# Kernel tuning notes

Measured on AMD Instinct MI355X. Metric: run time of the kernel, lower is better.

## Reference

```python
import jax, jax.numpy as jnp
import numpy as np

LAYER_SIZES = [1024, 1024, 1024, 1024, 1024, 1024, 512]
MAX_PATHS = 128
BATCH = 128
N_LAYERS = len(LAYER_SIZES) - 1


def setup_inputs() -> dict:
    key = jax.random.key(0)
    keys = jax.random.split(key, 1 + 2 * N_LAYERS)
    inp = {"x": jax.random.normal(keys[0], (BATCH, LAYER_SIZES[0]), dtype=jnp.float32)}
    for i in range(N_LAYERS):
        inp[f"W{i}"] = jax.random.normal(keys[1 + 2 * i], (LAYER_SIZES[i], LAYER_SIZES[i + 1]), dtype=jnp.float32) * 0.01
        inp[f"b{i}"] = jax.random.normal(keys[2 + 2 * i], (LAYER_SIZES[i + 1],), dtype=jnp.float32) * 0.01
    return inp


def _layer(data, W, b):
    # data: [B, in_feat, P] -> [B, out_feat, 3P]
    B, _, P = data.shape
    O = W.shape[1]
    pos = jnp.einsum('bfp,fo->bpo', data, W) + b          # [B, P, O]; neg branch is exactly -pos
    branches = jnp.stack([-pos, jnp.zeros_like(pos), pos], axis=-1)  # [B, P, O, 3]
    # transpose(1,2) then reshape: interleave branches per source path, matching torch
    return branches.transpose(0, 2, 1, 3).reshape(B, O, P * 3)


def _prune(data, keep):
    # keep top-`keep` paths by L2 norm over the feature dim
    norms = jnp.linalg.norm(data, axis=1)                 # [B, P]
    _, idx = jax.lax.top_k(norms, keep)                   # [B, keep]
    return jnp.take_along_axis(data, idx[:, None, :], axis=-1)


def _forward(x, Ws, bs):
    data = x[:, :, None]                                   # [B, F, 1]
    for i in range(N_LAYERS):
        data = _layer(data, Ws[i], bs[i])
        if i < N_LAYERS - 1:
            data = jnp.tanh(data)
        if data.shape[-1] > MAX_PATHS:
            data = _prune(data, MAX_PATHS)
    # collapse with 'max_abs': per (batch, feature) pick path with largest |value|
    idx = jnp.argmax(jnp.abs(data), axis=-1, keepdims=True)
    output = jnp.take_along_axis(data, idx, axis=-1).squeeze(-1)
    return output, data


def reference(x, W0, b0, W1, b1, W2, b2, W3, b3, W4, b4, W5, b5):
    Ws = [W0, W1, W2, W3, W4, W5]
    bs = [b0, b1, b2, b3, b4, b5]
    return _forward(x, Ws, bs)
```

## Files before the change

kernel.cpp:

```cpp
#include <hip/hip_runtime.h>
#include <math.h>


using s8v = __attribute__((ext_vector_type(8))) short;
using f4v = __attribute__((ext_vector_type(4))) float;

__device__ __forceinline__ float bf2f(short b) {
  unsigned u = ((unsigned)(unsigned short)b) << 16;
  return __builtin_bit_cast(float, u);
}
__device__ __forceinline__ short f2bf(float f) {
  unsigned u = __builtin_bit_cast(unsigned, f);
  u = (u + 0x7FFFu + ((u >> 16) & 1u)) >> 16;
  return (short)u;
}
__device__ __forceinline__ void split_store(float f, short* hi, short* lo) {
  short h = f2bf(f);
  *hi = h;
  *lo = f2bf(f - bf2f(h));
}

struct TWArgs {
  const float* W[6];
  short* Th[6];
  short* Tl[6];
};
__global__ void __launch_bounds__(256)
transW_all(TWArgs a, const float* __restrict__ x, short* __restrict__ A0h,
           short* __restrict__ A0l, float4* __restrict__ zreg) {
  __shared__ float tile[64][65];
  const int t = threadIdx.x;
  if (blockIdx.z == 6) {
    const int bf = blockIdx.y * 16 + blockIdx.x;
    if (bf < 128) {
      int i = (bf * 256 + t) * 4;
      float4 v = *(const float4*)&x[i];
      short4 h, l;
      h.x = f2bf(v.x); l.x = f2bf(v.x - bf2f(h.x));
      h.y = f2bf(v.y); l.y = f2bf(v.y - bf2f(h.y));
      h.z = f2bf(v.z); l.z = f2bf(v.z - bf2f(h.z));
      h.w = f2bf(v.w); l.w = f2bf(v.w - bf2f(h.w));
      *(short4*)&A0h[i] = h;
      *(short4*)&A0l[i] = l;
    } else {
      int flat = (bf - 128) * 256 + t;
      if (flat < 2976) {
        float4 zz = {0.f, 0.f, 0.f, 0.f};
        zreg[flat] = zz;
      }
    }
    return;
  }
  const int z = blockIdx.z;
  const int N = (z == 5) ? 512 : 1024;
  const int n0 = blockIdx.x * 64, k0 = blockIdx.y * 64;
  if (n0 >= N) return;
  const float* __restrict__ W = a.W[z];
  short* __restrict__ Th = a.Th[z];
  short* __restrict__ Tl = a.Tl[z];
  const int r = t >> 4, c4 = (t & 15) * 4;
#pragma unroll
  for (int i = 0; i < 4; ++i) {
    int rr = r + 16 * i;
    float4 v = *(const float4*)&W[(size_t)(k0 + rr) * N + n0 + c4];
    tile[rr][c4 + 0] = v.x;
    tile[rr][c4 + 1] = v.y;
    tile[rr][c4 + 2] = v.z;
    tile[rr][c4 + 3] = v.w;
  }
  __syncthreads();
#pragma unroll
  for (int i = 0; i < 4; ++i) {
    int n = r + 16 * i;
    short4 h, l;
    float f0 = tile[c4 + 0][n], f1 = tile[c4 + 1][n];
    float f2 = tile[c4 + 2][n], f3 = tile[c4 + 3][n];
    h.x = f2bf(f0); l.x = f2bf(f0 - bf2f(h.x));
    h.y = f2bf(f1); l.y = f2bf(f1 - bf2f(h.y));
    h.z = f2bf(f2); l.z = f2bf(f2 - bf2f(h.z));
    h.w = f2bf(f3); l.w = f2bf(f3 - bf2f(h.w));
    size_t o = (size_t)(n0 + n) * 1024 + k0 + c4;
    *(short4*)&Th[o] = h;
    *(short4*)&Tl[o] = l;
  }
}

template <int MODE, int D, int KS>
__device__ __forceinline__ void gemm_body(
    int bx, int by, int bz, int R, const short* __restrict__ Ah,
    const short* __restrict__ Al, const short* __restrict__ Bh,
    const short* __restrict__ Bl, const float* __restrict__ bias,
    short* __restrict__ Oh, short* __restrict__ Ol, float* __restrict__ Of,
    float* __restrict__ aux0, float* __restrict__ aux1, int N, int Dn) {
  constexpr int KC = 1024 / KS;
  constexpr int BKP = 40;
  __shared__ short As_h[64 * BKP], As_l[64 * BKP];
  __shared__ short Bs_h[64 * BKP], Bs_l[64 * BKP];
  const int t = threadIdx.x;
  const int row0 = by * 64;
  const int col0 = bx * 64;
  const int kb = bz * KC;
  const int sr = t >> 2, sko = (t & 3) * 8;
  const short* Ahp = Ah + (size_t)(row0 + sr) * 1024 + kb + sko;
  const short* Alp = Al + (size_t)(row0 + sr) * 1024 + kb + sko;
  const short* Bhp = Bh + (size_t)(col0 + sr) * 1024 + kb + sko;
  const short* Blp = Bl + (size_t)(col0 + sr) * 1024 + kb + sko;
  const int w = t >> 6, lane = t & 63;
  const int l16 = lane & 15, q = lane >> 4;
  const int wm0 = (w & 1) * 32, wn0 = (w >> 1) * 32;
  const int abase = (wm0 + l16) * BKP + q * 8;
  const int bbase = (wn0 + l16) * BKP + q * 8;
  f4v acc[2][2];
#pragma unroll
  for (int i = 0; i < 2; ++i)
#pragma unroll
    for (int j = 0; j < 2; ++j) acc[i][j] = (f4v){0.f, 0.f, 0.f, 0.f};
  uint4 rah = *(const uint4*)(Ahp);
  uint4 ral = *(const uint4*)(Alp);
  uint4 rbh = *(const uint4*)(Bhp);
  uint4 rbl = *(const uint4*)(Blp);
  for (int k0 = 0; k0 < KC; k0 += 32) {
    __syncthreads();
    *(uint4*)&As_h[sr * BKP + sko] = rah;
    *(uint4*)&As_l[sr * BKP + sko] = ral;
    *(uint4*)&Bs_h[sr * BKP + sko] = rbh;
    *(uint4*)&Bs_l[sr * BKP + sko] = rbl;
    if (k0 + 32 < KC) {
      rah = *(const uint4*)(Ahp + k0 + 32);
      ral = *(const uint4*)(Alp + k0 + 32);
      rbh = *(const uint4*)(Bhp + k0 + 32);
      rbl = *(const uint4*)(Blp + k0 + 32);
    }
    __syncthreads();
    s8v ah[2], al[2], bh[2], bl[2];
#pragma unroll
    for (int mt = 0; mt < 2; ++mt) {
      ah[mt] = *(const s8v*)&As_h[abase + mt * 16 * BKP];
      al[mt] = *(const s8v*)&As_l[abase + mt * 16 * BKP];
    }
#pragma unroll
    for (int nt = 0; nt < 2; ++nt) {
      bh[nt] = *(const s8v*)&Bs_h[bbase + nt * 16 * BKP];
      bl[nt] = *(const s8v*)&Bs_l[bbase + nt * 16 * BKP];
    }
#pragma unroll
    for (int mt = 0; mt < 2; ++mt)
#pragma unroll
      for (int nt = 0; nt < 2; ++nt) {
        acc[mt][nt] = __builtin_amdgcn_mfma_f32_16x16x32_bf16(
            ah[mt], bh[nt], acc[mt][nt], 0, 0, 0);
        acc[mt][nt] = __builtin_amdgcn_mfma_f32_16x16x32_bf16(
            ah[mt], bl[nt], acc[mt][nt], 0, 0, 0);
        acc[mt][nt] = __builtin_amdgcn_mfma_f32_16x16x32_bf16(
            al[mt], bh[nt], acc[mt][nt], 0, 0, 0);
      }
  }

  if (MODE == 1) {
    const float bc0 = bias[col0 + wn0 + l16];
    const float bc1 = bias[col0 + wn0 + 16 + l16];
#pragma unroll
    for (int mt = 0; mt < 2; ++mt) {
#pragma unroll
      for (int r = 0; r < 4; ++r) {
        const int rr = row0 + wm0 + mt * 16 + q * 4 + r;
        const int b = rr / D, u = rr - b * D;
        const size_t obr = (size_t)(b * Dn) * N;
        const size_t omr = obr + (size_t)(1 + 2 * u) * N;
        const size_t opr = obr + (size_t)(2 + 2 * u) * N;
        float sm = 0.f, sp = 0.f, sb = 0.f;
#pragma unroll
        for (int nt = 0; nt < 2; ++nt) {
          const int gcol = col0 + wn0 + nt * 16 + l16;
          const float bc = nt ? bc1 : bc0;
          const float v = acc[mt][nt][r];
          float tm = tanhf(bc - v), tp = tanhf(bc + v);
          split_store(tm, &Oh[omr + gcol], &Ol[omr + gcol]);
          split_store(tp, &Oh[opr + gcol], &Ol[opr + gcol]);
          sm = fmaf(tm, tm, sm);
          sp = fmaf(tp, tp, sp);
          if (u == 0) {
            float tb = tanhf(bc);
            split_store(tb, &Oh[obr + gcol], &Ol[obr + gcol]);
            sb = fmaf(tb, tb, sb);
          }
        }
#pragma unroll
        for (int d = 1; d < 16; d <<= 1) {
          sm += __shfl_xor(sm, d);
          sp += __shfl_xor(sp, d);
          sb += __shfl_xor(sb, d);
        }
        if (l16 == 0) {
          atomicAdd(&aux0[b * Dn + 1 + 2 * u], sm);
          atomicAdd(&aux0[b * Dn + 2 + 2 * u], sp);
          if (u == 0) atomicAdd(&aux0[b * Dn], sb);
        }
      }
    }
    return;
  }

  if (MODE == 2) {
    const float bc0 = bias[col0 + wn0 + l16];
    const float bc1 = bias[col0 + wn0 + 16 + l16];
#pragma unroll
    for (int mt = 0; mt < 2; ++mt) {
#pragma unroll
      for (int r = 0; r < 4; ++r) {
        const int rr = row0 + wm0 + mt * 16 + q * 4 + r;
        float sd = 0.f, sn = 0.f;
#pragma unroll
        for (int nt = 0; nt < 2; ++nt) {
          const int gcol = col0 + wn0 + nt * 16 + l16;
          const float bc = nt ? bc1 : bc0;
          const float v = acc[mt][nt][r];
          Of[(size_t)rr * N + gcol] = v;
          sd = fmaf(bc, v, sd);
          sn = fmaf(v, v, sn);
        }
#pragma unroll
        for (int d = 1; d < 16; d <<= 1) {
          sd += __shfl_xor(sd, d);
          sn += __shfl_xor(sn, d);
        }
        if (l16 == 0) {
          atomicAdd(&aux0[rr], sd);
          atomicAdd(&aux1[rr], sn);
        }
      }
    }
    return;
  }

#pragma unroll
  for (int nt = 0; nt < 2; ++nt) {
    int gcol = col0 + wn0 + nt * 16 + l16;
#pragma unroll
    for (int mt = 0; mt < 2; ++mt)
#pragma unroll
      for (int r = 0; r < 4; ++r) {
        int rr = row0 + wm0 + mt * 16 + q * 4 + r;
        Of[((size_t)bz * R + rr) * N + gcol] = acc[mt][nt][r];
      }
  }
}

template <int MODE, int D, int KS>
__global__ void __launch_bounds__(256, 2)
mfma_gemm(const short* __restrict__ Ah, const short* __restrict__ Al,
          const short* __restrict__ Bh, const short* __restrict__ Bl,
          const float* __restrict__ bias, short* __restrict__ Oh,
          short* __restrict__ Ol, float* __restrict__ Of,
          float* __restrict__ aux0, float* __restrict__ aux1, int N, int Dn) {
  gemm_body<MODE, D, KS>(blockIdx.x, blockIdx.y, blockIdx.z,
                         (int)gridDim.y << 6, Ah, Al, Bh, Bl, bias, Oh, Ol,
                         Of, aux0, aux1, N, Dn);
}

template <int KS>
__global__ void __launch_bounds__(256)
comb0_hl(const float* __restrict__ P, const float* __restrict__ bias,
         short* __restrict__ Oh, short* __restrict__ Ol, int R, int N) {
  int i = blockIdx.x * 256 + threadIdx.x;
  int n4 = N >> 2;
  int r = i / n4, c4 = (i - r * n4) * 4;
  float4 y = *(const float4*)&P[(size_t)r * N + c4];
  size_t stride = (size_t)R * N;
#pragma unroll
  for (int ks = 1; ks < KS; ++ks) {
    const float4 p = *(const float4*)&P[ks * stride + (size_t)r * N + c4];
    y.x += p.x; y.y += p.y; y.z += p.z; y.w += p.w;
  }
  float4 bc = *(const float4*)(bias + c4);
  float t0 = tanhf(bc.x + y.x), t1 = tanhf(bc.y + y.y);
  float t2 = tanhf(bc.z + y.z), t3 = tanhf(bc.w + y.w);
  short4 h, l;
  h.x = f2bf(t0); l.x = f2bf(t0 - bf2f(h.x));
  h.y = f2bf(t1); l.y = f2bf(t1 - bf2f(h.y));
  h.z = f2bf(t2); l.z = f2bf(t2 - bf2f(h.z));
  h.w = f2bf(t3); l.w = f2bf(t3 - bf2f(h.w));
  *(short4*)&Oh[(size_t)r * N + c4] = h;
  *(short4*)&Ol[(size_t)r * N + c4] = l;
}

template <int KS, int D>
__global__ void __launch_bounds__(256)
comb1_hl(const float* __restrict__ P, const float* __restrict__ bias,
         short* __restrict__ Oh, short* __restrict__ Ol, int R, int N,
         int Dn) {
  int i = blockIdx.x * 256 + threadIdx.x;
  int n4 = N >> 2;
  int r = i / n4, c4 = (i - r * n4) * 4;
  int b = r / D, u = r - b * D;
  float4 y = *(const float4*)&P[(size_t)r * N + c4];
  size_t stride = (size_t)R * N;
#pragma unroll
  for (int ks = 1; ks < KS; ++ks) {
    const float4 p = *(const float4*)&P[ks * stride + (size_t)r * N + c4];
    y.x += p.x; y.y += p.y; y.z += p.z; y.w += p.w;
  }
  float4 bc = *(const float4*)(bias + c4);
  size_t ob = (size_t)(b * Dn) * N + c4;
  size_t om = ob + (size_t)(1 + 2 * u) * N;
  size_t op = ob + (size_t)(2 + 2 * u) * N;
  {
    float t0 = tanhf(bc.x - y.x), t1 = tanhf(bc.y - y.y);
    float t2 = tanhf(bc.z - y.z), t3 = tanhf(bc.w - y.w);
    short4 h, l;
    h.x = f2bf(t0); l.x = f2bf(t0 - bf2f(h.x));
    h.y = f2bf(t1); l.y = f2bf(t1 - bf2f(h.y));
    h.z = f2bf(t2); l.z = f2bf(t2 - bf2f(h.z));
    h.w = f2bf(t3); l.w = f2bf(t3 - bf2f(h.w));
    *(short4*)&Oh[om] = h;
    *(short4*)&Ol[om] = l;
  }
  {
    float t0 = tanhf(bc.x + y.x), t1 = tanhf(bc.y + y.y);
    float t2 = tanhf(bc.z + y.z), t3 = tanhf(bc.w + y.w);
    short4 h, l;
    h.x = f2bf(t0); l.x = f2bf(t0 - bf2f(h.x));
    h.y = f2bf(t1); l.y = f2bf(t1 - bf2f(h.y));
    h.z = f2bf(t2); l.z = f2bf(t2 - bf2f(h.z));
    h.w = f2bf(t3); l.w = f2bf(t3 - bf2f(h.w));
    *(short4*)&Oh[op] = h;
    *(short4*)&Ol[op] = l;
  }
  if (u == 0) {
    float t0 = tanhf(bc.x), t1 = tanhf(bc.y);
    float t2 = tanhf(bc.z), t3 = tanhf(bc.w);
    short4 h, l;
    h.x = f2bf(t0); l.x = f2bf(t0 - bf2f(h.x));
    h.y = f2bf(t1); l.y = f2bf(t1 - bf2f(h.y));
    h.z = f2bf(t2); l.z = f2bf(t2 - bf2f(h.z));
    h.w = f2bf(t3); l.w = f2bf(t3 - bf2f(h.w));
    *(short4*)&Oh[ob] = h;
    *(short4*)&Ol[ob] = l;
  }
}

__global__ void __launch_bounds__(384)
prune45_k(const float* __restrict__ ns, const float* __restrict__ dotv,
          const float* __restrict__ nrmv, const float* __restrict__ b5,
          int* __restrict__ kept4, int* __restrict__ kept5) {
  const int b = blockIdx.x, t = threadIdx.x;
  __shared__ float nss[31];
  __shared__ float rb[256];
  __shared__ float keyA[243];
  __shared__ int cls[243];
  __shared__ int k4s[128];
  __shared__ float pns[128];
  __shared__ float keyB[384];
  if (t < 31) nss[t] = ns[b * 31 + t];
  if (t < 256) {
    float a = b5[t], c = b5[t + 256];
    rb[t] = fmaf(a, a, 0.f);
    rb[t] = fmaf(c, c, rb[t]);
  }
  __syncthreads();
  for (int off = 128; off; off >>= 1) {
    if (t < off) rb[t] += rb[t + off];
    __syncthreads();
  }
  const float nb5 = rb[0];
  if (t < 243) {
    int j = t / 3, t4 = t - 3 * j;
    int d0 = j / 27, d1 = (j / 9) % 3, d2 = (j / 3) % 3, d3 = j % 3;
    int u = 0;
    u = (d0 == 1) ? 0 : (1 + 2 * u + (d0 == 2));
    u = (d1 == 1) ? 0 : (1 + 2 * u + (d1 == 2));
    u = (d2 == 1) ? 0 : (1 + 2 * u + (d2 == 2));
    u = (d3 == 1) ? 0 : (1 + 2 * u + (d3 == 2));
    cls[t] = u;
    keyA[t] = (t4 == 1) ? 0.f : nss[u];
  }
  __syncthreads();
  if (t < 243) {
    float k = keyA[t];
    int rank = 0;
    for (int e = 0; e < 243; ++e) {
      float ke = keyA[e];
      rank += (ke > k) || (ke == k && e < t);
    }
    if (rank < 128) {
      int t4 = t - 3 * (t / 3);
      int kv = (cls[t] << 1) | (t4 == 2 ? 1 : 0);
      k4s[rank] = kv;
      kept4[b * 128 + rank] = kv;
    }
  }
  __syncthreads();
  if (t < 128) {
    int k4 = k4s[t];
    int c = k4 >> 1;
    float s = (k4 & 1) ? 1.f : -1.f;
    pns[t] = nb5 + nrmv[b * 31 + c] + s * 2.f * dotv[b * 31 + c];
  }
  __syncthreads();
  const int m = t / 3, tt = t - 3 * m;
  keyB[t] = (tt == 1) ? 0.f : pns[m];
  __syncthreads();
  float k = keyB[t];
  int rank = 0;
  for (int e = 0; e < 384; ++e) {
    float ke = keyB[e];
    rank += (ke > k) || (ke == k && e < t);
  }
  if (rank < 128) kept5[b * 128 + rank] = (m << 1) | (tt == 2 ? 1 : 0);
}

__global__ void __launch_bounds__(256)
finalize_k(const float* __restrict__ Y5, const float* __restrict__ b5,
           const int* __restrict__ kept4, const int* __restrict__ kept5,
           float* __restrict__ out, float* __restrict__ dataout) {
  const int b = blockIdx.y;
  const int o0 = blockIdx.x * 64;
  __shared__ float Ys[31][65];
  __shared__ float bias_s[64];
  __shared__ float vt[64][130];
  __shared__ float ra[64][4];
  __shared__ float rv[64][4];
  const int t = threadIdx.x;
  for (int idx = t; idx < 31 * 64; idx += 256) {
    int c = idx >> 6, o = idx & 63;
    Ys[c][o] = Y5[((size_t)b * 31 + c) * 512 + o0 + o];
  }
  if (t < 64) bias_s[t] = b5[o0 + t];
  const int rr = t & 127, oh = t >> 7;
  int k5 = kept5[b * 128 + rr];
  int m = k5 >> 1;
  float sig = (k5 & 1) ? 1.f : -1.f;
  int k4 = kept4[b * 128 + m];
  int cc = k4 >> 1;
  float s4 = (k4 & 1) ? 1.f : -1.f;
  float afac = sig * s4;
  __syncthreads();
#pragma unroll
  for (int ol = 0; ol < 32; ++ol) {
    int o = oh * 32 + ol;
    float v = sig * bias_s[o] + afac * Ys[cc][o];
    dataout[((size_t)b * 512 + o0 + o) * 128 + rr] = v;
    vt[o][rr] = v;
  }
  __syncthreads();
  int o = t >> 2, q = t & 3;
  float bestv = vt[o][q * 32];
  float besta = fabsf(bestv);
  for (int i = 1; i < 32; ++i) {
    float v = vt[o][q * 32 + i];
    float a = fabsf(v);
    if (a > besta) {
      besta = a;
      bestv = v;
    }
  }
  ra[o][q] = besta;
  rv[o][q] = bestv;
  __syncthreads();
  if (t < 64) {
    float ba = ra[t][0], bv = rv[t][0];
#pragma unroll
    for (int qq = 1; qq < 4; ++qq) {
      if (ra[t][qq] > ba) {
        ba = ra[t][qq];
        bv = rv[t][qq];
      }
    }
    out[(size_t)b * 512 + o0 + t] = bv;
  }
}

extern "C" void kernel_launch(void* const* d_in, const int* in_sizes, int n_in,
                              void* d_out, int out_size, void* d_ws,
                              size_t ws_size, hipStream_t stream) {
  const float* x = (const float*)d_in[0];
  const float* Wt[6];
  const float* bs[6];
  for (int i = 0; i < 6; ++i) {
    Wt[i] = (const float*)d_in[1 + 2 * i];
    bs[i] = (const float*)d_in[2 + 2 * i];
  }
  char* base = (char*)d_ws;
  short* A0h = (short*)(base + 0);
  short* A0l = (short*)(base + 262144);
  short* Wh[6], *Wl[6];
  {
    size_t off = 524288;
    for (int i = 0; i < 6; ++i) {
      size_t sz = (i < 5) ? 2097152 : 1048576;
      Wh[i] = (short*)(base + off);
      Wl[i] = (short*)(base + off + sz);
      off += 2 * sz;
    }
  }
  short* C1h = (short*)(base + 23592960), *C1l = (short*)(base + 23855104);
  short* C2h = (short*)(base + 24117248), *C2l = (short*)(base + 24903680);
  short* C3h = (short*)(base + 25690112), *C3l = (short*)(base + 27525120);
  short* C4h = (short*)(base + 29360128), *C4l = (short*)(base + 33292288);
  short* C5h = (short*)(base + 524288);
  short* C5l = (short*)(base + 8912896);
  float* PA = (float*)(base + 29360128);
  float* PB = (float*)(base + 524288);
  float* Y5 = (float*)(base + 23592960);
  char* zb = base + 37224448;
  float* ns = (float*)zb;
  float* dotv = (float*)(zb + 15872);
  float* nrmv = (float*)(zb + 31744);
  int* kept4 = (int*)(zb + 47616);
  int* kept5 = (int*)(zb + 113152);
  float* outp = (float*)d_out;
  float* dataout = outp + 128 * 512;

  dim3 blk(256);
  TWArgs twa;
  for (int i = 0; i < 6; ++i) {
    twa.W[i] = Wt[i];
    twa.Th[i] = Wh[i];
    twa.Tl[i] = Wl[i];
  }
  transW_all<<<dim3(16, 16, 7), blk, 0, stream>>>(twa, x, A0h, A0l,
                                                  (float4*)zb);
  mfma_gemm<3, 1, 8><<<dim3(16, 2, 8), blk, 0, stream>>>(
      A0h, A0l, Wh[0], Wl[0], nullptr, nullptr, nullptr, PA, nullptr, nullptr,
      1024, 0);
  comb0_hl<8><<<dim3(128), blk, 0, stream>>>(PA, bs[0], C1h, C1l, 128, 1024);
  mfma_gemm<3, 1, 8><<<dim3(16, 2, 8), blk, 0, stream>>>(
      C1h, C1l, Wh[1], Wl[1], nullptr, nullptr, nullptr, PA, nullptr, nullptr,
      1024, 0);
  comb1_hl<8, 1><<<dim3(128), blk, 0, stream>>>(PA, bs[1], C2h, C2l, 128, 1024,
                                                3);
  mfma_gemm<3, 3, 4><<<dim3(16, 6, 4), blk, 0, stream>>>(
      C2h, C2l, Wh[2], Wl[2], nullptr, nullptr, nullptr, PA, nullptr, nullptr,
      1024, 0);
  comb1_hl<4, 3><<<dim3(384), blk, 0, stream>>>(PA, bs[2], C3h, C3l, 384, 1024,
                                                7);
  mfma_gemm<3, 7, 2><<<dim3(16, 14, 2), blk, 0, stream>>>(
      C3h, C3l, Wh[3], Wl[3], nullptr, nullptr, nullptr, PB, nullptr, nullptr,
      1024, 0);
  comb1_hl<2, 7><<<dim3(896), blk, 0, stream>>>(PB, bs[3], C4h, C4l, 896, 1024,
                                                15);
  mfma_gemm<1, 15, 1><<<dim3(16, 30), blk, 0, stream>>>(
      C4h, C4l, Wh[4], Wl[4], bs[4], C5h, C5l, nullptr, ns, nullptr, 1024, 31);
  mfma_gemm<2, 31, 1><<<dim3(8, 62), blk, 0, stream>>>(
      C5h, C5l, Wh[5], Wl[5], bs[5], nullptr, nullptr, Y5, dotv, nrmv, 512, 0);
  prune45_k<<<dim3(128), dim3(384), 0, stream>>>(ns, dotv, nrmv, bs[5], kept4,
                                                 kept5);
  finalize_k<<<dim3(8, 128), blk, 0, stream>>>(Y5, bs[5], kept4, kept5, outp,
                                               dataout);
}
```

Baseline: 241.6 us.

## Move layer-4 path norms from atomic epilogue into row-norm blocks fused with GEMM5

The layer-4 GEMM epilogue no longer computes squared norms with shuffle reductions and atomics. Those norms are now computed by extra blocks appended to the layer-5 GEMM launch, which re-read the hi/lo bf16 output rows and reduce them in shared memory. The goal is a lighter layer-4 epilogue with no atomic contention, at the cost of roughly 3968 extra small blocks that re-read about 16 MB of activations. The zero-init region shrinks because ns no longer needs clearing.

```diff
diff --git a/kernel.cpp b/kernel.cpp
--- a/kernel.cpp
+++ b/kernel.cpp
@@ -44,7 +44,7 @@
       *(short4*)&A0l[i] = l;
     } else {
       int flat = (bf - 128) * 256 + t;
-      if (flat < 2976) {
+      if (flat < 1984) {
         float4 zz = {0.f, 0.f, 0.f, 0.f};
         zreg[flat] = zz;
       }
@@ -156,51 +156,6 @@
       }
   }
 
-  if (MODE == 1) {
-    const float bc0 = bias[col0 + wn0 + l16];
-    const float bc1 = bias[col0 + wn0 + 16 + l16];
-#pragma unroll
-    for (int mt = 0; mt < 2; ++mt) {
-#pragma unroll
-      for (int r = 0; r < 4; ++r) {
-        const int rr = row0 + wm0 + mt * 16 + q * 4 + r;
-        const int b = rr / D, u = rr - b * D;
-        const size_t obr = (size_t)(b * Dn) * N;
-        const size_t omr = obr + (size_t)(1 + 2 * u) * N;
-        const size_t opr = obr + (size_t)(2 + 2 * u) * N;
-        float sm = 0.f, sp = 0.f, sb = 0.f;
-#pragma unroll
-        for (int nt = 0; nt < 2; ++nt) {
-          const int gcol = col0 + wn0 + nt * 16 + l16;
-          const float bc = nt ? bc1 : bc0;
-          const float v = acc[mt][nt][r];
-          float tm = tanhf(bc - v), tp = tanhf(bc + v);
-          split_store(tm, &Oh[omr + gcol], &Ol[omr + gcol]);
-          split_store(tp, &Oh[opr + gcol], &Ol[opr + gcol]);
-          sm = fmaf(tm, tm, sm);
-          sp = fmaf(tp, tp, sp);
-          if (u == 0) {
-            float tb = tanhf(bc);
-            split_store(tb, &Oh[obr + gcol], &Ol[obr + gcol]);
-            sb = fmaf(tb, tb, sb);
-          }
-        }
-#pragma unroll
-        for (int d = 1; d < 16; d <<= 1) {
-          sm += __shfl_xor(sm, d);
-          sp += __shfl_xor(sp, d);
-          sb += __shfl_xor(sb, d);
-        }
-        if (l16 == 0) {
-          atomicAdd(&aux0[b * Dn + 1 + 2 * u], sm);
-          atomicAdd(&aux0[b * Dn + 2 + 2 * u], sp);
-          if (u == 0) atomicAdd(&aux0[b * Dn], sb);
-        }
-      }
-    }
-    return;
-  }
-
   if (MODE == 2) {
     const float bc0 = bias[col0 + wn0 + l16];
     const float bc1 = bias[col0 + wn0 + 16 + l16];
@@ -236,13 +191,26 @@
 #pragma unroll
   for (int nt = 0; nt < 2; ++nt) {
     int gcol = col0 + wn0 + nt * 16 + l16;
-#pragma unroll
-    for (int mt = 0; mt < 2; ++mt)
+    float bc = (MODE == 1) ? bias[gcol] : 0.f;
+#pragma unroll
+    for (int mt = 0; mt < 2; ++mt) {
 #pragma unroll
       for (int r = 0; r < 4; ++r) {
+        float v = acc[mt][nt][r];
         int rr = row0 + wm0 + mt * 16 + q * 4 + r;
-        Of[((size_t)bz * R + rr) * N + gcol] = acc[mt][nt][r];
+        if (MODE == 1) {
+          int b = rr / D, u = rr - b * D;
+          size_t ob = (size_t)(b * Dn) * N + gcol;
+          size_t om = ob + (size_t)(1 + 2 * u) * N;
+          size_t op = ob + (size_t)(2 + 2 * u) * N;
+          split_store(tanhf(bc - v), &Oh[om], &Ol[om]);
+          split_store(tanhf(bc + v), &Oh[op], &Ol[op]);
+          if (u == 0) split_store(tanhf(bc), &Oh[ob], &Ol[ob]);
+        } else {
+          Of[((size_t)bz * R + rr) * N + gcol] = v;
+        }
       }
+    }
   }
 }
 
@@ -256,6 +224,43 @@
   gemm_body<MODE, D, KS>(blockIdx.x, blockIdx.y, blockIdx.z,
                          (int)gridDim.y << 6, Ah, Al, Bh, Bl, bias, Oh, Ol,
                          Of, aux0, aux1, N, Dn);
+}
+
+__device__ __forceinline__ void rownorm_body(const short* __restrict__ hi,
+                                             const short* __restrict__ lo,
+                                             float* __restrict__ ns, int row) {
+  int t = threadIdx.x;
+  size_t base = (size_t)row * 1024 + t * 4;
+  short4 h = *(const short4*)&hi[base];
+  short4 l = *(const short4*)&lo[base];
+  float v0 = bf2f(h.x) + bf2f(l.x);
+  float v1 = bf2f(h.y) + bf2f(l.y);
+  float v2 = bf2f(h.z) + bf2f(l.z);
+  float v3 = bf2f(h.w) + bf2f(l.w);
+  float s = v0 * v0 + v1 * v1 + v2 * v2 + v3 * v3;
+  __shared__ float red[256];
+  red[t] = s;
+  __syncthreads();
+  for (int off = 128; off; off >>= 1) {
+    if (t < off) red[t] += red[t + off];
+    __syncthreads();
+  }
+  if (t == 0) ns[row] = red[0];
+}
+
+__global__ void __launch_bounds__(256, 2)
+gemm5_rownorm(const short* __restrict__ C5h, const short* __restrict__ C5l,
+              const short* __restrict__ W5h, const short* __restrict__ W5l,
+              const float* __restrict__ b5, float* __restrict__ Y5,
+              float* __restrict__ ns, float* __restrict__ dotv,
+              float* __restrict__ nrmv) {
+  const int bid = blockIdx.x;
+  if (bid < 496) {
+    gemm_body<2, 31, 1>(bid & 7, bid >> 3, 0, 0, C5h, C5l, W5h, W5l, b5,
+                        nullptr, nullptr, Y5, dotv, nrmv, 512, 0);
+  } else {
+    rownorm_body(C5h, C5l, ns, bid - 496);
+  }
 }
 
 template <int KS>
@@ -503,9 +508,9 @@
   float* PB = (float*)(base + 524288);
   float* Y5 = (float*)(base + 23592960);
   char* zb = base + 37224448;
-  float* ns = (float*)zb;
-  float* dotv = (float*)(zb + 15872);
-  float* nrmv = (float*)(zb + 31744);
+  float* dotv = (float*)zb;
+  float* nrmv = (float*)(zb + 15872);
+  float* ns = (float*)(zb + 31744);
   int* kept4 = (int*)(zb + 47616);
   int* kept5 = (int*)(zb + 113152);
   float* outp = (float*)d_out;
@@ -540,9 +545,10 @@
   comb1_hl<2, 7><<<dim3(896), blk, 0, stream>>>(PB, bs[3], C4h, C4l, 896, 1024,
                                                 15);
   mfma_gemm<1, 15, 1><<<dim3(16, 30), blk, 0, stream>>>(
-      C4h, C4l, Wh[4], Wl[4], bs[4], C5h, C5l, nullptr, ns, nullptr, 1024, 31);
-  mfma_gemm<2, 31, 1><<<dim3(8, 62), blk, 0, stream>>>(
-      C5h, C5l, Wh[5], Wl[5], bs[5], nullptr, nullptr, Y5, dotv, nrmv, 512, 0);
+      C4h, C4l, Wh[4], Wl[4], bs[4], C5h, C5l, nullptr, nullptr, nullptr, 1024,
+      31);
+  gemm5_rownorm<<<dim3(496 + 3968), blk, 0, stream>>>(
+      C5h, C5l, Wh[5], Wl[5], bs[5], Y5, ns, dotv, nrmv);
   prune45_k<<<dim3(128), dim3(384), 0, stream>>>(ns, dotv, nrmv, bs[5], kept4,
                                                  kept5);
   finalize_k<<<dim3(8, 128), blk, 0, stream>>>(Y5, bs[5], kept4, kept5, outp,
```

Measured after the change: 232.6 us (median of 2 runs). 1.04x faster.
